# Performance work log

Measured on AMD Instinct MI355X. Metric: run time of the kernel, lower is better.

Reference implementation:

```python
import jax, jax.numpy as jnp
import numpy as np
from jax import lax

N = 500_000
D = 128            # in_channels
B = 8192           # number of graphs (segments)
T = 6              # processing_steps


def setup_inputs() -> dict:
    key = jax.random.key(0)
    k1, k2, k3, k4, k5, k6 = jax.random.split(key, 6)
    x = jax.random.normal(k1, (N, D), dtype=jnp.float32)
    batch = jnp.sort(jax.random.randint(k2, (N,), 0, B)).astype(jnp.int64)
    s = 1.0 / np.sqrt(D)  # torch LSTM init scale: U(-1/sqrt(hidden), 1/sqrt(hidden))
    W_ih = jax.random.uniform(k3, (4 * D, 2 * D), jnp.float32, -s, s)
    W_hh = jax.random.uniform(k4, (4 * D, D), jnp.float32, -s, s)
    b_ih = jax.random.uniform(k5, (4 * D,), jnp.float32, -s, s)
    b_hh = jax.random.uniform(k6, (4 * D,), jnp.float32, -s, s)
    return {"x": x, "batch": batch, "W_ih": W_ih, "W_hh": W_hh,
            "b_ih": b_ih, "b_hh": b_hh}


def reference(x, batch, W_ih, W_hh, b_ih, b_hh):
    d = x.shape[1]
    h0 = jnp.zeros((B, d), x.dtype)
    c0 = jnp.zeros((B, d), x.dtype)
    q_star0 = jnp.zeros((B, 2 * d), x.dtype)

    def step(carry, _):
        h, c, q_star = carry
        # single-layer torch LSTM cell on seq of length 1
        gates = q_star @ W_ih.T + b_ih + h @ W_hh.T + b_hh  # [B, 4d]
        i, f, g, o = jnp.split(gates, 4, axis=-1)
        i = jax.nn.sigmoid(i)
        f = jax.nn.sigmoid(f)
        g = jnp.tanh(g)
        o = jax.nn.sigmoid(o)
        c = f * c + i * g
        h = o * jnp.tanh(c)
        q = h  # [B, d]
        # attention logits per node
        e = jnp.sum(x * q[batch], axis=-1)  # [N]
        # segment-wise stable softmax (PyG softmax semantics)
        e_max = jax.ops.segment_max(e, batch, num_segments=B)
        ex = jnp.exp(e - e_max[batch])
        denom = jax.ops.segment_sum(ex, batch, num_segments=B)
        a = ex / (denom[batch] + 1e-16)  # [N]
        # scatter-add readout
        r = jax.ops.segment_sum(a[:, None] * x, batch, num_segments=B)  # [B, d]
        q_star = jnp.concatenate([q, r], axis=-1)
        return (h, c, q_star), None

    (h, c, q_star), _ = lax.scan(step, (h0, c0, q_star0), None, length=T)
    return q_star
```

## Files before the change

kernel.cpp:

```cpp
#include <hip/hip_runtime.h>
#include <hip/hip_bf16.h>
#include <cstddef>
#include <cstdint>

#define NNODES 500000
#define DIM    128
#define NSEG   8192
#define TSTEPS 6

typedef __attribute__((ext_vector_type(8))) short bf16x8;
typedef __attribute__((ext_vector_type(4))) float f32x4;
typedef unsigned short ushort_t;

static __device__ inline ushort_t f2bf_u(float f) {
    __hip_bfloat16 h = __float2bfloat16(f);
    return *reinterpret_cast<ushort_t*>(&h);
}
static __device__ inline float bfu2f(ushort_t u) {
    union { unsigned i; float f; } c; c.i = ((unsigned)u) << 16; return c.f;
}

__global__ void seg_bounds_k(const int* __restrict__ batch, int* __restrict__ seg, int n) {
    int b = blockIdx.x * blockDim.x + threadIdx.x;
    if (b > NSEG) return;
    int lo = 0, hi = n;
    while (lo < hi) {
        int mid = (lo + hi) >> 1;
        if (batch[mid] < b) lo = mid + 1; else hi = mid;
    }
    seg[b] = lo;
}

__global__ __launch_bounds__(256) void wconv_k(
    const float* __restrict__ Wih, const float* __restrict__ Whh,
    __hip_bfloat16* __restrict__ wbuf)
{
    int idx = blockIdx.x * 256 + threadIdx.x;
    int n = idx / 384, k = idx - n * 384;
    float v = (k < 256) ? Wih[n * 256 + k] : Whh[n * 128 + (k - 256)];
    wbuf[idx] = __float2bfloat16(v);
}

__global__ __launch_bounds__(256) void gemm_mfma_k(
    const __hip_bfloat16* __restrict__ abuf,
    const __hip_bfloat16* __restrict__ wbuf,
    float* __restrict__ gates)
{
    __shared__ char As[128 * 128];
    __shared__ char Bs[64 * 128];
    const int tid  = threadIdx.x;
    const int lane = tid & 63, wave = tid >> 6;
    const int wrow = (wave >> 1) * 64;
    const int wcol = (wave & 1) * 32;
    const int m0 = blockIdx.y * 128;
    const int n0 = blockIdx.x * 64;

    const int ar  = tid >> 1;
    const int acb = (tid & 1) * 64;
    const int br  = tid >> 2;
    const int bcb = (tid & 3) * 32;

    const char* aP = (const char*)(abuf + (size_t)(m0 + ar) * 384) + acb;
    const char* bP = (const char*)(wbuf + (size_t)(n0 + br) * 384) + bcb;

    f32x4 acc[4][2] = {};

    int4 ra[4]; int4 rb2[2];
    #pragma unroll
    for (int c = 0; c < 4; ++c) ra[c]  = *(const int4*)(aP + c * 16);
    #pragma unroll
    for (int c = 0; c < 2; ++c) rb2[c] = *(const int4*)(bP + c * 16);

    char* asw = As + ar * 128;
    char* bsw = Bs + br * 128;
    const int amask = (ar & 7) << 4;
    const int bmask = (br & 7) << 4;

    for (int s = 0; s < 6; ++s) {
        __syncthreads();
        #pragma unroll
        for (int c = 0; c < 4; ++c)
            *(int4*)(asw + ((acb + c * 16) ^ amask)) = ra[c];
        #pragma unroll
        for (int c = 0; c < 2; ++c)
            *(int4*)(bsw + ((bcb + c * 16) ^ bmask)) = rb2[c];
        __syncthreads();

        if (s < 5) {
            const char* aN = aP + (size_t)(s + 1) * 128;
            const char* bN = bP + (size_t)(s + 1) * 128;
            #pragma unroll
            for (int c = 0; c < 4; ++c) ra[c]  = *(const int4*)(aN + c * 16);
            #pragma unroll
            for (int c = 0; c < 2; ++c) rb2[c] = *(const int4*)(bN + c * 16);
        }

        #pragma unroll
        for (int ks = 0; ks < 2; ++ks) {
            const int kb = ks * 64 + ((lane >> 4) << 4);
            bf16x8 af[4], bfr[2];
            #pragma unroll
            for (int rbk = 0; rbk < 4; ++rbk) {
                int r = wrow + rbk * 16 + (lane & 15);
                af[rbk] = *(const bf16x8*)(As + r * 128 + (kb ^ ((r & 7) << 4)));
            }
            #pragma unroll
            for (int cb = 0; cb < 2; ++cb) {
                int n = wcol + cb * 16 + (lane & 15);
                bfr[cb] = *(const bf16x8*)(Bs + n * 128 + (kb ^ ((n & 7) << 4)));
            }
            #pragma unroll
            for (int rbk = 0; rbk < 4; ++rbk)
                #pragma unroll
                for (int cb = 0; cb < 2; ++cb)
                    acc[rbk][cb] = __builtin_amdgcn_mfma_f32_16x16x32_bf16(
                        af[rbk], bfr[cb], acc[rbk][cb], 0, 0, 0);
        }
    }

    const int rowb = (lane >> 4) << 2;
    const int coll = lane & 15;
    #pragma unroll
    for (int rbk = 0; rbk < 4; ++rbk)
        #pragma unroll
        for (int cb = 0; cb < 2; ++cb) {
            int row = m0 + wrow + rbk * 16 + rowb;
            int col = n0 + wcol + cb * 16 + coll;
            float* gp = gates + (size_t)row * 512 + col;
            #pragma unroll
            for (int reg = 0; reg < 4; ++reg)
                gp[(size_t)reg * 512] = acc[rbk][cb][reg];
        }
}

__global__ __launch_bounds__(128) void attn_lstm_k(
    const float* __restrict__ x, ushort_t* __restrict__ xbf,
    const int* __restrict__ seg, const float* __restrict__ gates,
    const float* __restrict__ bih, const float* __restrict__ bhh,
    float* __restrict__ cbuf, float* __restrict__ qstar,
    __hip_bfloat16* __restrict__ abuf,
    int t0, int read_bf, int write_bf)
{
    const int tid  = threadIdx.x;
    const int wv   = tid >> 6, lane = tid & 63;
    const int b    = blockIdx.x;
    const int l16  = lane & 15;
    const int ggrp = (wv << 2) | (lane >> 4);

    __shared__ float hsh[128];
    __shared__ float gm[8], gden[8];
    __shared__ float racc_s[8][128];

    {
        const int d = tid;
        float gi, gf, gg, go;
        if (t0) {
            gi = bih[d]       + bhh[d];
            gf = bih[128 + d] + bhh[128 + d];
            gg = bih[256 + d] + bhh[256 + d];
            go = bih[384 + d] + bhh[384 + d];
        } else {
            const float* g = gates + (size_t)b * 512;
            gi = g[d]       + bih[d]       + bhh[d];
            gf = g[128 + d] + bih[128 + d] + bhh[128 + d];
            gg = g[256 + d] + bih[256 + d] + bhh[256 + d];
            go = g[384 + d] + bih[384 + d] + bhh[384 + d];
        }
        float iv = 1.f / (1.f + expf(-gi));
        float fv = 1.f / (1.f + expf(-gf));
        float gv = tanhf(gg);
        float ov = 1.f / (1.f + expf(-go));
        float cp = t0 ? 0.f : cbuf[(size_t)b * 128 + d];
        float c  = fv * cp + iv * gv;
        float h  = ov * tanhf(c);
        cbuf[(size_t)b * 128 + d] = c;
        qstar[(size_t)b * 256 + d] = h;
        __hip_bfloat16 hb = __float2bfloat16(h);
        abuf[(size_t)b * 384 + d] = hb;
        abuf[(size_t)b * 384 + 256 + d] = hb;
        hsh[d] = h;
    }
    __syncthreads();

    const int ns = seg[b], ne = seg[b + 1];
    if (ns >= ne) {
        qstar[(size_t)b * 256 + DIM + tid] = 0.f;
        abuf[(size_t)b * 384 + 128 + tid] = __float2bfloat16(0.f);
        return;
    }

    float hreg[8];
    #pragma unroll
    for (int i = 0; i < 8; ++i) hreg[i] = hsh[8 * l16 + i];

    float m = -INFINITY, den = 0.f;
    float racc[8] = {};

    if (read_bf) {
        int j = ns + ggrp;
        if (j < ne) {
            int4 v = *(const int4*)(xbf + (size_t)j * 128 + 8 * l16);
            for (int jn = j + 8; ; jn += 8) {
                const bool more = (jn < ne);
                int4 vn;
                if (more) vn = *(const int4*)(xbf + (size_t)jn * 128 + 8 * l16);
                const ushort_t* u = (const ushort_t*)&v;
                float xv[8];
                #pragma unroll
                for (int i = 0; i < 8; ++i) xv[i] = bfu2f(u[i]);
                float s = xv[0]*hreg[0] + xv[1]*hreg[1] + xv[2]*hreg[2] + xv[3]*hreg[3]
                        + xv[4]*hreg[4] + xv[5]*hreg[5] + xv[6]*hreg[6] + xv[7]*hreg[7];
                s += __shfl_xor(s, 1); s += __shfl_xor(s, 2);
                s += __shfl_xor(s, 4); s += __shfl_xor(s, 8);
                const float mn = fmaxf(m, s);
                const float scale = expf(m - mn);
                const float w = expf(s - mn);
                den = den * scale + w;
                #pragma unroll
                for (int i = 0; i < 8; ++i) racc[i] = fmaf(racc[i], scale, w * xv[i]);
                m = mn;
                if (!more) break;
                v = vn;
            }
        }
    } else {
        int j = ns + ggrp;
        if (j < ne) {
            const float4* xp = (const float4*)(x + (size_t)j * DIM + 8 * l16);
            float4 va = xp[0], vb = xp[1];
            for (int jn = j + 8; ; jn += 8) {
                const bool more = (jn < ne);
                float4 na, nb;
                if (more) {
                    const float4* xn = (const float4*)(x + (size_t)jn * DIM + 8 * l16);
                    na = xn[0]; nb = xn[1];
                }
                float xv[8] = {va.x, va.y, va.z, va.w, vb.x, vb.y, vb.z, vb.w};
                if (write_bf) {
                    int4 pk;
                    unsigned* pu = (unsigned*)&pk;
                    pu[0] = (unsigned)f2bf_u(xv[0]) | ((unsigned)f2bf_u(xv[1]) << 16);
                    pu[1] = (unsigned)f2bf_u(xv[2]) | ((unsigned)f2bf_u(xv[3]) << 16);
                    pu[2] = (unsigned)f2bf_u(xv[4]) | ((unsigned)f2bf_u(xv[5]) << 16);
                    pu[3] = (unsigned)f2bf_u(xv[6]) | ((unsigned)f2bf_u(xv[7]) << 16);
                    *(int4*)(xbf + (size_t)(jn - 8) * 128 + 8 * l16) = pk;
                }
                float s = xv[0]*hreg[0] + xv[1]*hreg[1] + xv[2]*hreg[2] + xv[3]*hreg[3]
                        + xv[4]*hreg[4] + xv[5]*hreg[5] + xv[6]*hreg[6] + xv[7]*hreg[7];
                s += __shfl_xor(s, 1); s += __shfl_xor(s, 2);
                s += __shfl_xor(s, 4); s += __shfl_xor(s, 8);
                const float mn = fmaxf(m, s);
                const float scale = expf(m - mn);
                const float w = expf(s - mn);
                den = den * scale + w;
                #pragma unroll
                for (int i = 0; i < 8; ++i) racc[i] = fmaf(racc[i], scale, w * xv[i]);
                m = mn;
                if (!more) break;
                va = na; vb = nb;
            }
        }
    }

    if (l16 == 0) { gm[ggrp] = m; gden[ggrp] = den; }
    *(float4*)&racc_s[ggrp][8 * l16]     = make_float4(racc[0], racc[1], racc[2], racc[3]);
    *(float4*)&racc_s[ggrp][8 * l16 + 4] = make_float4(racc[4], racc[5], racc[6], racc[7]);
    __syncthreads();

    {
        float mM = gm[0];
        #pragma unroll
        for (int g = 1; g < 8; ++g) mM = fmaxf(mM, gm[g]);
        float dtot = 0.f, rtot = 0.f;
        #pragma unroll
        for (int g = 0; g < 8; ++g) {
            const float k = expf(gm[g] - mM);
            dtot = fmaf(k, gden[g], dtot);
            rtot = fmaf(k, racc_s[g][tid], rtot);
        }
        const float rv = rtot / (dtot + 1e-16f);
        qstar[(size_t)b * 256 + DIM + tid] = rv;
        abuf[(size_t)b * 384 + 128 + tid] = __float2bfloat16(rv);
    }
}

extern "C" void kernel_launch(void* const* d_in, const int* in_sizes, int n_in,
                              void* d_out, int out_size, void* d_ws, size_t ws_size,
                              hipStream_t stream) {
    const float* x     = (const float*)d_in[0];
    const int*   batch = (const int*)d_in[1];
    const float* Wih   = (const float*)d_in[2];
    const float* Whh   = (const float*)d_in[3];
    const float* bih   = (const float*)d_in[4];
    const float* bhh   = (const float*)d_in[5];
    float* out = (float*)d_out;

    float* cbuf  = (float*)d_ws;
    float* gates = cbuf + (size_t)NSEG * DIM;
    __hip_bfloat16* abuf = (__hip_bfloat16*)(gates + (size_t)NSEG * 512);
    __hip_bfloat16* wbuf = abuf + (size_t)NSEG * 384;
    int* seg = (int*)(wbuf + (size_t)512 * 384);
    size_t fixed_bytes = (size_t)((char*)(seg + NSEG + 1) - (char*)d_ws);
    size_t xbf_off = (fixed_bytes + 15) & ~(size_t)15;
    ushort_t* xbf = (ushort_t*)((char*)d_ws + xbf_off);
    size_t need = xbf_off + (size_t)NNODES * DIM * sizeof(ushort_t);
    const int use_xbf = (ws_size >= need) ? 1 : 0;

    seg_bounds_k<<<(NSEG + 256) / 256, 256, 0, stream>>>(batch, seg, NNODES);
    wconv_k<<<(512 * 384) / 256, 256, 0, stream>>>(Wih, Whh, wbuf);

    dim3 ggrid(512 / 64, NSEG / 128);
    for (int t = 0; t < TSTEPS; ++t) {
        if (t > 0)
            gemm_mfma_k<<<ggrid, 256, 0, stream>>>(abuf, wbuf, gates);
        const int read_bf  = (use_xbf && t > 0) ? 1 : 0;
        const int write_bf = (use_xbf && t == 0) ? 1 : 0;
        attn_lstm_k<<<NSEG, 128, 0, stream>>>(x, xbf, seg, gates, bih, bhh,
                                              cbuf, out, abuf,
                                              (t == 0) ? 1 : 0, read_bf, write_bf);
    }
}
```

Before: 394.5 us.

## Fuse all Set2Set steps into one persistent kernel per 16-segment block

```diff
diff --git a/kernel.cpp b/kernel.cpp
--- a/kernel.cpp
+++ b/kernel.cpp
@@ -7,6 +7,7 @@
 #define DIM    128
 #define NSEG   8192
 #define TSTEPS 6
+#define SEGB   16
 
 typedef __attribute__((ext_vector_type(8))) short bf16x8;
 typedef __attribute__((ext_vector_type(4))) float f32x4;
@@ -41,246 +42,171 @@
     wbuf[idx] = __float2bfloat16(v);
 }
 
-__global__ __launch_bounds__(256) void gemm_mfma_k(
-    const __hip_bfloat16* __restrict__ abuf,
-    const __hip_bfloat16* __restrict__ wbuf,
-    float* __restrict__ gates)
+__global__ __launch_bounds__(256) void set2set_mega_k(
+    const float* __restrict__ x, ushort_t* __restrict__ xbf,
+    const int* __restrict__ seg_arr, const __hip_bfloat16* __restrict__ wbuf,
+    const float* __restrict__ bih, const float* __restrict__ bhh,
+    float* __restrict__ qstar, int use_xbf)
 {
-    __shared__ char As[128 * 128];
-    __shared__ char Bs[64 * 128];
-    const int tid  = threadIdx.x;
-    const int lane = tid & 63, wave = tid >> 6;
-    const int wrow = (wave >> 1) * 64;
-    const int wcol = (wave & 1) * 32;
-    const int m0 = blockIdx.y * 128;
-    const int n0 = blockIdx.x * 64;
-
-    const int ar  = tid >> 1;
-    const int acb = (tid & 1) * 64;
-    const int br  = tid >> 2;
-    const int bcb = (tid & 3) * 32;
-
-    const char* aP = (const char*)(abuf + (size_t)(m0 + ar) * 384) + acb;
-    const char* bP = (const char*)(wbuf + (size_t)(n0 + br) * 384) + bcb;
-
-    f32x4 acc[4][2] = {};
-
-    int4 ra[4]; int4 rb2[2];
-    #pragma unroll
-    for (int c = 0; c < 4; ++c) ra[c]  = *(const int4*)(aP + c * 16);
-    #pragma unroll
-    for (int c = 0; c < 2; ++c) rb2[c] = *(const int4*)(bP + c * 16);
-
-    char* asw = As + ar * 128;
-    char* bsw = Bs + br * 128;
-    const int amask = (ar & 7) << 4;
-    const int bmask = (br & 7) << 4;
-
-    for (int s = 0; s < 6; ++s) {
-        __syncthreads();
-        #pragma unroll
-        for (int c = 0; c < 4; ++c)
-            *(int4*)(asw + ((acb + c * 16) ^ amask)) = ra[c];
-        #pragma unroll
-        for (int c = 0; c < 2; ++c)
-            *(int4*)(bsw + ((bcb + c * 16) ^ bmask)) = rb2[c];
-        __syncthreads();
-
-        if (s < 5) {
-            const char* aN = aP + (size_t)(s + 1) * 128;
-            const char* bN = bP + (size_t)(s + 1) * 128;
-            #pragma unroll
-            for (int c = 0; c < 4; ++c) ra[c]  = *(const int4*)(aN + c * 16);
-            #pragma unroll
-            for (int c = 0; c < 2; ++c) rb2[c] = *(const int4*)(bN + c * 16);
-        }
-
-        #pragma unroll
-        for (int ks = 0; ks < 2; ++ks) {
-            const int kb = ks * 64 + ((lane >> 4) << 4);
-            bf16x8 af[4], bfr[2];
-            #pragma unroll
-            for (int rbk = 0; rbk < 4; ++rbk) {
-                int r = wrow + rbk * 16 + (lane & 15);
-                af[rbk] = *(const bf16x8*)(As + r * 128 + (kb ^ ((r & 7) << 4)));
-            }
-            #pragma unroll
-            for (int cb = 0; cb < 2; ++cb) {
-                int n = wcol + cb * 16 + (lane & 15);
-                bfr[cb] = *(const bf16x8*)(Bs + n * 128 + (kb ^ ((n & 7) << 4)));
-            }
-            #pragma unroll
-            for (int rbk = 0; rbk < 4; ++rbk)
-                #pragma unroll
-                for (int cb = 0; cb < 2; ++cb)
-                    acc[rbk][cb] = __builtin_amdgcn_mfma_f32_16x16x32_bf16(
-                        af[rbk], bfr[cb], acc[rbk][cb], 0, 0, 0);
-        }
-    }
-
-    const int rowb = (lane >> 4) << 2;
-    const int coll = lane & 15;
-    #pragma unroll
-    for (int rbk = 0; rbk < 4; ++rbk)
-        #pragma unroll
-        for (int cb = 0; cb < 2; ++cb) {
-            int row = m0 + wrow + rbk * 16 + rowb;
-            int col = n0 + wcol + cb * 16 + coll;
-            float* gp = gates + (size_t)row * 512 + col;
-            #pragma unroll
-            for (int reg = 0; reg < 4; ++reg)
-                gp[(size_t)reg * 512] = acc[rbk][cb][reg];
-        }
-}
-
-__global__ __launch_bounds__(128) void attn_lstm_k(
-    const float* __restrict__ x, ushort_t* __restrict__ xbf,
-    const int* __restrict__ seg, const float* __restrict__ gates,
-    const float* __restrict__ bih, const float* __restrict__ bhh,
-    float* __restrict__ cbuf, float* __restrict__ qstar,
-    __hip_bfloat16* __restrict__ abuf,
-    int t0, int read_bf, int write_bf)
-{
+    __shared__ ushort_t Ash[SEGB][392];
+    __shared__ float    hsh[SEGB][128];
+    __shared__ float    bsh[512];
+
     const int tid  = threadIdx.x;
     const int wv   = tid >> 6, lane = tid & 63;
-    const int b    = blockIdx.x;
-    const int l16  = lane & 15;
-    const int ggrp = (wv << 2) | (lane >> 4);
-
-    __shared__ float hsh[128];
-    __shared__ float gm[8], gden[8];
-    __shared__ float racc_s[8][128];
-
-    {
-        const int d = tid;
-        float gi, gf, gg, go;
-        if (t0) {
-            gi = bih[d]       + bhh[d];
-            gf = bih[128 + d] + bhh[128 + d];
-            gg = bih[256 + d] + bhh[256 + d];
-            go = bih[384 + d] + bhh[384 + d];
-        } else {
-            const float* g = gates + (size_t)b * 512;
-            gi = g[d]       + bih[d]       + bhh[d];
-            gf = g[128 + d] + bih[128 + d] + bhh[128 + d];
-            gg = g[256 + d] + bih[256 + d] + bhh[256 + d];
-            go = g[384 + d] + bih[384 + d] + bhh[384 + d];
-        }
-        float iv = 1.f / (1.f + expf(-gi));
-        float fv = 1.f / (1.f + expf(-gf));
-        float gv = tanhf(gg);
-        float ov = 1.f / (1.f + expf(-go));
-        float cp = t0 ? 0.f : cbuf[(size_t)b * 128 + d];
-        float c  = fv * cp + iv * gv;
-        float h  = ov * tanhf(c);
-        cbuf[(size_t)b * 128 + d] = c;
-        qstar[(size_t)b * 256 + d] = h;
-        __hip_bfloat16 hb = __float2bfloat16(h);
-        abuf[(size_t)b * 384 + d] = hb;
-        abuf[(size_t)b * 384 + 256 + d] = hb;
-        hsh[d] = h;
-    }
+    const int l16  = lane & 15, k8 = lane >> 4;
+    const int s0   = blockIdx.x * SEGB;
+    const int g    = tid >> 4;
+    const int segb = s0 + g;
+    const int ns   = seg_arr[segb], ne = seg_arr[segb + 1];
+
+    for (int i = tid; i < 512; i += 256) bsh[i] = bih[i] + bhh[i];
+
+    float creg[8];
+    #pragma unroll
+    for (int i = 0; i < 8; ++i) creg[i] = 0.f;
+
     __syncthreads();
 
-    const int ns = seg[b], ne = seg[b + 1];
-    if (ns >= ne) {
-        qstar[(size_t)b * 256 + DIM + tid] = 0.f;
-        abuf[(size_t)b * 384 + 128 + tid] = __float2bfloat16(0.f);
-        return;
-    }
-
-    float hreg[8];
-    #pragma unroll
-    for (int i = 0; i < 8; ++i) hreg[i] = hsh[8 * l16 + i];
-
-    float m = -INFINITY, den = 0.f;
-    float racc[8] = {};
-
-    if (read_bf) {
-        int j = ns + ggrp;
-        if (j < ne) {
-            int4 v = *(const int4*)(xbf + (size_t)j * 128 + 8 * l16);
-            for (int jn = j + 8; ; jn += 8) {
-                const bool more = (jn < ne);
-                int4 vn;
-                if (more) vn = *(const int4*)(xbf + (size_t)jn * 128 + 8 * l16);
-                const ushort_t* u = (const ushort_t*)&v;
-                float xv[8];
+    for (int t = 0; t < TSTEPS; ++t) {
+        f32x4 acc[4][2];
+        if (t > 0) {
+            #pragma unroll
+            for (int gg2 = 0; gg2 < 4; ++gg2)
                 #pragma unroll
-                for (int i = 0; i < 8; ++i) xv[i] = bfu2f(u[i]);
-                float s = xv[0]*hreg[0] + xv[1]*hreg[1] + xv[2]*hreg[2] + xv[3]*hreg[3]
-                        + xv[4]*hreg[4] + xv[5]*hreg[5] + xv[6]*hreg[6] + xv[7]*hreg[7];
-                s += __shfl_xor(s, 1); s += __shfl_xor(s, 2);
-                s += __shfl_xor(s, 4); s += __shfl_xor(s, 8);
-                const float mn = fmaxf(m, s);
-                const float scale = expf(m - mn);
-                const float w = expf(s - mn);
-                den = den * scale + w;
+                for (int c2 = 0; c2 < 2; ++c2)
+                    acc[gg2][c2] = (f32x4){0.f, 0.f, 0.f, 0.f};
+            #pragma unroll
+            for (int ks = 0; ks < 12; ++ks) {
+                bf16x8 af = *(const bf16x8*)&Ash[l16][ks * 32 + k8 * 8];
                 #pragma unroll
-                for (int i = 0; i < 8; ++i) racc[i] = fmaf(racc[i], scale, w * xv[i]);
-                m = mn;
-                if (!more) break;
-                v = vn;
+                for (int gg2 = 0; gg2 < 4; ++gg2)
+                    #pragma unroll
+                    for (int c2 = 0; c2 < 2; ++c2) {
+                        const int n = gg2 * 128 + wv * 32 + c2 * 16 + l16;
+                        bf16x8 bf = *(const bf16x8*)((const ushort_t*)wbuf
+                                     + (size_t)n * 384 + ks * 32 + k8 * 8);
+                        acc[gg2][c2] = __builtin_amdgcn_mfma_f32_16x16x32_bf16(
+                            af, bf, acc[gg2][c2], 0, 0, 0);
+                    }
             }
         }
-    } else {
-        int j = ns + ggrp;
-        if (j < ne) {
-            const float4* xp = (const float4*)(x + (size_t)j * DIM + 8 * l16);
-            float4 va = xp[0], vb = xp[1];
-            for (int jn = j + 8; ; jn += 8) {
-                const bool more = (jn < ne);
-                float4 na, nb;
-                if (more) {
-                    const float4* xn = (const float4*)(x + (size_t)jn * DIM + 8 * l16);
-                    na = xn[0]; nb = xn[1];
+        __syncthreads();
+
+        #pragma unroll
+        for (int c2 = 0; c2 < 2; ++c2) {
+            const int d = 32 * wv + 16 * c2 + l16;
+            const float b0 = bsh[d], b1 = bsh[128 + d], b2 = bsh[256 + d], b3 = bsh[384 + d];
+            #pragma unroll
+            for (int reg = 0; reg < 4; ++reg) {
+                const int s = 4 * k8 + reg;
+                float gi = b0, gf = b1, gg = b2, go = b3;
+                if (t > 0) {
+                    gi += acc[0][c2][reg]; gf += acc[1][c2][reg];
+                    gg += acc[2][c2][reg]; go += acc[3][c2][reg];
                 }
-                float xv[8] = {va.x, va.y, va.z, va.w, vb.x, vb.y, vb.z, vb.w};
-                if (write_bf) {
-                    int4 pk;
-                    unsigned* pu = (unsigned*)&pk;
-                    pu[0] = (unsigned)f2bf_u(xv[0]) | ((unsigned)f2bf_u(xv[1]) << 16);
-                    pu[1] = (unsigned)f2bf_u(xv[2]) | ((unsigned)f2bf_u(xv[3]) << 16);
-                    pu[2] = (unsigned)f2bf_u(xv[4]) | ((unsigned)f2bf_u(xv[5]) << 16);
-                    pu[3] = (unsigned)f2bf_u(xv[6]) | ((unsigned)f2bf_u(xv[7]) << 16);
-                    *(int4*)(xbf + (size_t)(jn - 8) * 128 + 8 * l16) = pk;
+                const float iv = 1.f / (1.f + expf(-gi));
+                const float fv = 1.f / (1.f + expf(-gf));
+                const float gv = tanhf(gg);
+                const float ov = 1.f / (1.f + expf(-go));
+                const float c  = fv * creg[reg * 2 + c2] + iv * gv;
+                const float h  = ov * tanhf(c);
+                creg[reg * 2 + c2] = c;
+                hsh[s][d] = h;
+                const ushort_t hb = f2bf_u(h);
+                Ash[s][d] = hb;
+                Ash[s][256 + d] = hb;
+                if (t == TSTEPS - 1) qstar[(size_t)(s0 + s) * 256 + d] = h;
+            }
+        }
+        __syncthreads();
+
+        float hreg[8];
+        #pragma unroll
+        for (int i = 0; i < 8; ++i) hreg[i] = hsh[g][8 * l16 + i];
+
+        float m = -INFINITY, den = 0.f;
+        float racc[8] = {0.f, 0.f, 0.f, 0.f, 0.f, 0.f, 0.f, 0.f};
+        const int read_bf = (use_xbf && t > 0) ? 1 : 0;
+
+        if (ns < ne) {
+            if (read_bf) {
+                int4 v = *(const int4*)(xbf + (size_t)ns * DIM + 8 * l16);
+                for (int j = ns; j < ne; ++j) {
+                    int4 vn;
+                    if (j + 1 < ne) vn = *(const int4*)(xbf + (size_t)(j + 1) * DIM + 8 * l16);
+                    const ushort_t* u = (const ushort_t*)&v;
+                    float xv[8];
+                    #pragma unroll
+                    for (int i = 0; i < 8; ++i) xv[i] = bfu2f(u[i]);
+                    float sd = xv[0]*hreg[0] + xv[1]*hreg[1] + xv[2]*hreg[2] + xv[3]*hreg[3]
+                             + xv[4]*hreg[4] + xv[5]*hreg[5] + xv[6]*hreg[6] + xv[7]*hreg[7];
+                    sd += __shfl_xor(sd, 1); sd += __shfl_xor(sd, 2);
+                    sd += __shfl_xor(sd, 4); sd += __shfl_xor(sd, 8);
+                    const float mn = fmaxf(m, sd);
+                    const float sc = expf(m - mn);
+                    const float w  = expf(sd - mn);
+                    den = den * sc + w;
+                    #pragma unroll
+                    for (int i = 0; i < 8; ++i) racc[i] = fmaf(racc[i], sc, w * xv[i]);
+                    m = mn;
+                    v = vn;
                 }
-                float s = xv[0]*hreg[0] + xv[1]*hreg[1] + xv[2]*hreg[2] + xv[3]*hreg[3]
-                        + xv[4]*hreg[4] + xv[5]*hreg[5] + xv[6]*hreg[6] + xv[7]*hreg[7];
-                s += __shfl_xor(s, 1); s += __shfl_xor(s, 2);
-                s += __shfl_xor(s, 4); s += __shfl_xor(s, 8);
-                const float mn = fmaxf(m, s);
-                const float scale = expf(m - mn);
-                const float w = expf(s - mn);
-                den = den * scale + w;
-                #pragma unroll
-                for (int i = 0; i < 8; ++i) racc[i] = fmaf(racc[i], scale, w * xv[i]);
-                m = mn;
-                if (!more) break;
-                va = na; vb = nb;
+            } else {
+                const int do_wb = (use_xbf && t == 0) ? 1 : 0;
+                const float4* xp = (const float4*)(x + (size_t)ns * DIM + 8 * l16);
+                float4 va = xp[0], vb = xp[1];
+                for (int j = ns; j < ne; ++j) {
+                    float4 na, nb;
+                    if (j + 1 < ne) {
+                        const float4* xn = (const float4*)(x + (size_t)(j + 1) * DIM + 8 * l16);
+                        na = xn[0]; nb = xn[1];
+                    }
+                    float xv[8] = {va.x, va.y, va.z, va.w, vb.x, vb.y, vb.z, vb.w};
+                    if (do_wb) {
+                        int4 pk;
+                        unsigned* pu = (unsigned*)&pk;
+                        pu[0] = (unsigned)f2bf_u(xv[0]) | ((unsigned)f2bf_u(xv[1]) << 16);
+                        pu[1] = (unsigned)f2bf_u(xv[2]) | ((unsigned)f2bf_u(xv[3]) << 16);
+                        pu[2] = (unsigned)f2bf_u(xv[4]) | ((unsigned)f2bf_u(xv[5]) << 16);
+                        pu[3] = (unsigned)f2bf_u(xv[6]) | ((unsigned)f2bf_u(xv[7]) << 16);
+                        *(int4*)(xbf + (size_t)j * DIM + 8 * l16) = pk;
+                    }
+                    float sd = xv[0]*hreg[0] + xv[1]*hreg[1] + xv[2]*hreg[2] + xv[3]*hreg[3]
+                             + xv[4]*hreg[4] + xv[5]*hreg[5] + xv[6]*hreg[6] + xv[7]*hreg[7];
+                    sd += __shfl_xor(sd, 1); sd += __shfl_xor(sd, 2);
+                    sd += __shfl_xor(sd, 4); sd += __shfl_xor(sd, 8);
+                    const float mn = fmaxf(m, sd);
+                    const float sc = expf(m - mn);
+                    const float w  = expf(sd - mn);
+                    den = den * sc + w;
+                    #pragma unroll
+                    for (int i = 0; i < 8; ++i) racc[i] = fmaf(racc[i], sc, w * xv[i]);
+                    m = mn;
+                    va = na; vb = nb;
+                }
             }
         }
-    }
-
-    if (l16 == 0) { gm[ggrp] = m; gden[ggrp] = den; }
-    *(float4*)&racc_s[ggrp][8 * l16]     = make_float4(racc[0], racc[1], racc[2], racc[3]);
-    *(float4*)&racc_s[ggrp][8 * l16 + 4] = make_float4(racc[4], racc[5], racc[6], racc[7]);
-    __syncthreads();
-
-    {
-        float mM = gm[0];
+
+        const float rden = 1.f / (den + 1e-16f);
+        float rv[8];
         #pragma unroll
-        for (int g = 1; g < 8; ++g) mM = fmaxf(mM, gm[g]);
-        float dtot = 0.f, rtot = 0.f;
-        #pragma unroll
-        for (int g = 0; g < 8; ++g) {
-            const float k = expf(gm[g] - mM);
-            dtot = fmaf(k, gden[g], dtot);
-            rtot = fmaf(k, racc_s[g][tid], rtot);
-        }
-        const float rv = rtot / (dtot + 1e-16f);
-        qstar[(size_t)b * 256 + DIM + tid] = rv;
-        abuf[(size_t)b * 384 + 128 + tid] = __float2bfloat16(rv);
+        for (int i = 0; i < 8; ++i) rv[i] = racc[i] * rden;
+        {
+            int4 pk;
+            unsigned* pu = (unsigned*)&pk;
+            #pragma unroll
+            for (int i = 0; i < 4; ++i)
+                pu[i] = (unsigned)f2bf_u(rv[2 * i]) | ((unsigned)f2bf_u(rv[2 * i + 1]) << 16);
+            *(int4*)&Ash[g][128 + 8 * l16] = pk;
+        }
+        if (t == TSTEPS - 1) {
+            *(float4*)(qstar + (size_t)segb * 256 + DIM + 8 * l16)
+                = make_float4(rv[0], rv[1], rv[2], rv[3]);
+            *(float4*)(qstar + (size_t)segb * 256 + DIM + 8 * l16 + 4)
+                = make_float4(rv[4], rv[5], rv[6], rv[7]);
+        }
+        __syncthreads();
     }
 }
 
@@ -295,10 +221,7 @@
     const float* bhh   = (const float*)d_in[5];
     float* out = (float*)d_out;
 
-    float* cbuf  = (float*)d_ws;
-    float* gates = cbuf + (size_t)NSEG * DIM;
-    __hip_bfloat16* abuf = (__hip_bfloat16*)(gates + (size_t)NSEG * 512);
-    __hip_bfloat16* wbuf = abuf + (size_t)NSEG * 384;
+    __hip_bfloat16* wbuf = (__hip_bfloat16*)d_ws;
     int* seg = (int*)(wbuf + (size_t)512 * 384);
     size_t fixed_bytes = (size_t)((char*)(seg + NSEG + 1) - (char*)d_ws);
     size_t xbf_off = (fixed_bytes + 15) & ~(size_t)15;
@@ -309,14 +232,6 @@
     seg_bounds_k<<<(NSEG + 256) / 256, 256, 0, stream>>>(batch, seg, NNODES);
     wconv_k<<<(512 * 384) / 256, 256, 0, stream>>>(Wih, Whh, wbuf);
 
-    dim3 ggrid(512 / 64, NSEG / 128);
-    for (int t = 0; t < TSTEPS; ++t) {
-        if (t > 0)
-            gemm_mfma_k<<<ggrid, 256, 0, stream>>>(abuf, wbuf, gates);
-        const int read_bf  = (use_xbf && t > 0) ? 1 : 0;
-        const int write_bf = (use_xbf && t == 0) ? 1 : 0;
-        attn_lstm_k<<<NSEG, 128, 0, stream>>>(x, xbf, seg, gates, bih, bhh,
-                                              cbuf, out, abuf,
-                                              (t == 0) ? 1 : 0, read_bf, write_bf);
-    }
-}
+    set2set_mega_k<<<NSEG / SEGB, 256, 0, stream>>>(x, xbf, seg, wbuf,
+                                                    bih, bhh, out, use_xbf);
+}
```

After: 854.0 us. +116.5%, slower.
